# Kernel optimization log

Measured on AMD Instinct MI355X. Metric: run time of the kernel, lower is better.

## Reference

```python
import jax, jax.numpy as jnp
import numpy as np

T, D, E, F, K = 2048, 1024, 16, 512, 2  # tokens, hidden, experts, expert d_ff, top_k
NORM_TOPK = True


def setup_inputs() -> dict:
    key = jax.random.key(0)
    k0, k1, k2, k3 = jax.random.split(key, 4)
    hidden_states = jax.random.normal(k0, (T, D), jnp.float32)
    w_gate = jax.random.normal(k1, (E, D), jnp.float32) * (D ** -0.5)      # router Linear(D, E), no bias
    w13 = jax.random.normal(k2, (E, 2 * F, D), jnp.float32) * (D ** -0.5)  # fused gate+up proj per expert
    w2 = jax.random.normal(k3, (E, D, F), jnp.float32) * (F ** -0.5)       # down proj per expert
    return {"hidden_states": hidden_states, "w_gate": w_gate, "w13": w13, "w2": w2}


def reference(hidden_states, w_gate, w13, w2):
    # Router: softmax (fp32) -> top-k -> optional renorm
    logits = hidden_states @ w_gate.T                                   # [T, E]
    probs = jax.nn.softmax(logits.astype(jnp.float32), axis=-1)
    weights, selected = jax.lax.top_k(probs, K)                          # [T, K]
    if NORM_TOPK:
        weights = weights / jnp.sum(weights, axis=-1, keepdims=True)
    weights = weights.astype(hidden_states.dtype)

    # Sparse combine matrix: combine[t, e] = routing weight iff expert e selected for token t
    combine = jnp.zeros((T, E), hidden_states.dtype)
    combine = combine.at[jnp.arange(T)[:, None], selected].add(weights)

    # Expert FFN (computed for all experts, zeroed by combine; faithful math)
    h = jnp.einsum('td,efd->tef', hidden_states, w13)                    # [T, E, 2F]
    gate, up = jnp.split(h, 2, axis=-1)
    act = jax.nn.silu(gate) * up                                         # SiluAndMul, [T, E, F]
    y = jnp.einsum('tef,edf->ted', act, w2)                              # [T, E, D]
    return jnp.einsum('ted,te->td', y, combine)                          # [T, D]
```

## Files before the change

### kernel.cpp

```cpp
#include <hip/hip_runtime.h>
#include <hip/hip_bf16.h>
#include <math.h>

#define T_TOK 2048
#define DIM   1024
#define NEXP  16
#define FDIM  512
#define TOPK  2

#define BM 128
#define BN 64
#define BK 32

typedef float f32x4 __attribute__((ext_vector_type(4)));
typedef short s16x8 __attribute__((ext_vector_type(8)));

static __device__ __forceinline__ ushort f2bf(float f) {
  union { float f; unsigned u; } v; v.f = f;
  unsigned u = v.u;
  unsigned r = u + 0x7fffu + ((u >> 16) & 1u);
  return (ushort)(r >> 16);
}
static __device__ __forceinline__ float bf2f(ushort h) {
  union { unsigned u; float f; } v; v.u = ((unsigned)h) << 16; return v.f;
}
static __device__ __forceinline__ void split2(float f, ushort& h, ushort& l) {
  ushort hb = f2bf(f);
  h = hb;
  l = f2bf(f - bf2f(hb));
}

__global__ __launch_bounds__(64) void router_k(const float* __restrict__ x,
                                               const float* __restrict__ wg,
                                               int* __restrict__ sel,
                                               float* __restrict__ wt,
                                               int* __restrict__ cnt) {
  int t = blockIdx.x;
  int lane = threadIdx.x;
  const float* xr = x + (size_t)t * DIM;
  float acc[NEXP];
#pragma unroll
  for (int e = 0; e < NEXP; ++e) acc[e] = 0.f;
  for (int d0 = 0; d0 < DIM; d0 += 64) {
    float xv = xr[d0 + lane];
#pragma unroll
    for (int e = 0; e < NEXP; ++e) acc[e] += xv * wg[e * DIM + d0 + lane];
  }
#pragma unroll
  for (int e = 0; e < NEXP; ++e) {
    float v = acc[e];
    v += __shfl_xor(v, 32); v += __shfl_xor(v, 16); v += __shfl_xor(v, 8);
    v += __shfl_xor(v, 4);  v += __shfl_xor(v, 2);  v += __shfl_xor(v, 1);
    acc[e] = v;
  }
  if (lane == 0) {
    float b1 = -1e30f, b2 = -1e30f; int i1 = 0, i2 = 0;
#pragma unroll
    for (int e = 0; e < NEXP; ++e) {
      float v = acc[e];
      if (v > b1) { b2 = b1; i2 = i1; b1 = v; i1 = e; }
      else if (v > b2) { b2 = v; i2 = e; }
    }
    float r = expf(b2 - b1);
    float w2v = r / (1.f + r);
    float w1v = 1.f - w2v;
    sel[t * 2 + 0] = i1; sel[t * 2 + 1] = i2;
    wt[t * 2 + 0] = w1v; wt[t * 2 + 1] = w2v;
    atomicAdd(&cnt[i1], 1);
    atomicAdd(&cnt[i2], 1);
  }
}

__global__ __launch_bounds__(256) void xsplit_k(const float* __restrict__ x,
                                                ushort* __restrict__ xhi,
                                                ushort* __restrict__ xlo) {
  int idx = (blockIdx.x * 256 + threadIdx.x) * 4;
  float4 v = *(const float4*)(x + idx);
  ushort h0,h1,h2,h3,l0,l1,l2,l3;
  split2(v.x, h0, l0); split2(v.y, h1, l1);
  split2(v.z, h2, l2); split2(v.w, h3, l3);
  *(ushort4*)(xhi + idx) = make_ushort4(h0, h1, h2, h3);
  *(ushort4*)(xlo + idx) = make_ushort4(l0, l1, l2, l3);
}

__global__ void offsets_k(const int* __restrict__ cnt, int* __restrict__ off) {
  if (threadIdx.x == 0 && blockIdx.x == 0) {
    int s = 0;
#pragma unroll
    for (int e = 0; e < NEXP; ++e) { off[e] = s; s += cnt[e]; }
    off[NEXP] = s;
  }
}

__global__ __launch_bounds__(256) void fill_k(const int* __restrict__ sel,
                                              const float* __restrict__ wt,
                                              const int* __restrict__ off,
                                              int* __restrict__ cnt2,
                                              int* __restrict__ rowtok,
                                              float* __restrict__ rowwt) {
  int i = blockIdx.x * 256 + threadIdx.x;
  if (i >= T_TOK * TOPK) return;
  int e = sel[i];
  int pos = off[e] + atomicAdd(&cnt2[e], 1);
  rowtok[pos] = i >> 1;
  rowwt[pos] = wt[i];
}

#define DECL_SET(S) uint4 pAh0##S, pAl0##S, pAh1##S, pAl1##S; float4 pB0##S, pB1##S;

#define LOAD_SET(S, KB)                                                      \
  pAh0##S = *(const uint4*)(a0h + (KB)); pAl0##S = *(const uint4*)(a0l + (KB)); \
  pAh1##S = *(const uint4*)(a1h + (KB)); pAl1##S = *(const uint4*)(a1l + (KB)); \
  pB0##S = *(const float4*)(bsrc + (KB)); pB1##S = *(const float4*)(bsrc + (KB) + 4);

#define MOE_KSTEP(S, KS, NSv)                                                \
  do {                                                                       \
    asm volatile("s_waitcnt lgkmcnt(0)" ::: "memory");   \
    __builtin_amdgcn_s_barrier();               \
    __builtin_amdgcn_sched_barrier(0);                                       \
    *(uint4*)((char*)Ah + boA0) = pAh0##S;                                   \
    *(uint4*)((char*)Al + boA0) = pAl0##S;                                   \
    *(uint4*)((char*)Ah + boA1) = pAh1##S;                                   \
    *(uint4*)((char*)Al + boA1) = pAl1##S;                                   \
    {                                                                        \
      float fv[8] = {pB0##S.x, pB0##S.y, pB0##S.z, pB0##S.w,                 \
                     pB1##S.x, pB1##S.y, pB1##S.z, pB1##S.w};                \
      uint hp[4], lp[4];                                                     \
      _Pragma("unroll")                                                      \
      for (int j = 0; j < 4; ++j) {                                          \
        ushort ha, la, hb, lb;                                               \
        split2(fv[2 * j], ha, la);                                           \
        split2(fv[2 * j + 1], hb, lb);                                       \
        hp[j] = (uint)ha | ((uint)hb << 16);                                 \
        lp[j] = (uint)la | ((uint)lb << 16);                                 \
      }                                                                      \
      *(uint4*)((char*)Bh + boB) = make_uint4(hp[0], hp[1], hp[2], hp[3]);   \
      *(uint4*)((char*)Bl + boB) = make_uint4(lp[0], lp[1], lp[2], lp[3]);   \
    }                                                                        \
    if ((KS) + 2 < (NSv)) { int kb = ((KS) + 2) * BK; LOAD_SET(S, kb) }      \
    asm volatile("s_waitcnt lgkmcnt(0)" ::: "memory");  \
    __builtin_amdgcn_s_barrier();             \
    __builtin_amdgcn_sched_barrier(0);                                       \
    s16x8 ah[4], al[4], bh[2], bl[2];                                        \
    _Pragma("unroll")                                                        \
    for (int fm = 0; fm < 4; ++fm) {                                         \
      int row = wm + fm * 16 + lr;                                           \
      int bo = (row * 64 + lk * 16) ^ ((row & 7) << 4);                      \
      ah[fm] = *(const s16x8*)((char*)Ah + bo);                              \
      al[fm] = *(const s16x8*)((char*)Al + bo);                              \
    }                                                                        \
    _Pragma("unroll")                                                        \
    for (int fn = 0; fn < 2; ++fn) {                                         \
      int row = wn + fn * 16 + lr;                                           \
      int bo = (row * 64 + lk * 16) ^ ((row & 7) << 4);                      \
      bh[fn] = *(const s16x8*)((char*)Bh + bo);                              \
      bl[fn] = *(const s16x8*)((char*)Bl + bo);                              \
    }                                                                        \
    _Pragma("unroll")                                                        \
    for (int fm = 0; fm < 4; ++fm)                                           \
      _Pragma("unroll")                                                      \
      for (int fn = 0; fn < 2; ++fn) {                                       \
        acc[fm][fn] = __builtin_amdgcn_mfma_f32_16x16x32_bf16(ah[fm], bh[fn], acc[fm][fn], 0, 0, 0); \
        acc[fm][fn] = __builtin_amdgcn_mfma_f32_16x16x32_bf16(ah[fm], bl[fn], acc[fm][fn], 0, 0, 0); \
        acc[fm][fn] = __builtin_amdgcn_mfma_f32_16x16x32_bf16(al[fm], bh[fn], acc[fm][fn], 0, 0, 0); \
      }                                                                      \
  } while (0)

__global__ __launch_bounds__(256, 2) void gemm1_k(const ushort* __restrict__ xhi,
                                                  const ushort* __restrict__ xlo,
                                                  const float* __restrict__ w13,
                                                  const int* __restrict__ off,
                                                  const int* __restrict__ rowtok,
                                                  float* __restrict__ H) {
  int e = blockIdx.z;
  int rbeg = off[e];
  int rows = off[e + 1] - rbeg;
  int m0 = blockIdx.y * BM;
  if (m0 >= rows) return;
  int n0 = blockIdx.x * BN;

  __shared__ ushort Ah[BM * BK], Al[BM * BK], Bh[BN * BK], Bl[BN * BK];
  __shared__ int toksh[BM];

  int tid = threadIdx.x;
  if (tid < BM) {
    int r = m0 + tid;
    toksh[tid] = rowtok[rbeg + (r < rows ? r : rows - 1)];
  }
  __syncthreads();

  int srow = tid >> 2;
  int sc = tid & 3;
  int tok0 = toksh[srow];
  int tok1 = toksh[srow + 64];
  const ushort* a0h = xhi + (size_t)tok0 * DIM + sc * 8;
  const ushort* a0l = xlo + (size_t)tok0 * DIM + sc * 8;
  const ushort* a1h = xhi + (size_t)tok1 * DIM + sc * 8;
  const ushort* a1l = xlo + (size_t)tok1 * DIM + sc * 8;
  const float*  bsrc = w13 + ((size_t)e * (2 * FDIM) + (n0 + srow)) * DIM + sc * 8;

  int boA0 = (srow * 64 + sc * 16) ^ ((srow & 7) << 4);
  int boA1 = ((srow + 64) * 64 + sc * 16) ^ ((srow & 7) << 4);
  int boB  = boA0;

  f32x4 acc[4][2];
#pragma unroll
  for (int a = 0; a < 4; ++a)
#pragma unroll
    for (int b = 0; b < 2; ++b) acc[a][b] = {0.f, 0.f, 0.f, 0.f};

  int lane = tid & 63;
  int w = tid >> 6;
  int wm = (w & 1) * 64, wn = (w >> 1) * 32;
  int lr = lane & 15, lk = lane >> 4;

  DECL_SET(_A) DECL_SET(_B)
  LOAD_SET(_A, 0)
  LOAD_SET(_B, BK)

  const int NS = DIM / BK;
  for (int ks = 0; ks < NS; ks += 2) {
    MOE_KSTEP(_A, ks, NS);
    MOE_KSTEP(_B, ks + 1, NS);
  }

#pragma unroll
  for (int fm = 0; fm < 4; ++fm) {
    int rloc = wm + fm * 16 + lk * 4;
#pragma unroll
    for (int j = 0; j < 4; ++j) {
      int row = rloc + j;
      if (m0 + row < rows) {
        size_t gr = (size_t)(rbeg + m0 + row) * (2 * FDIM);
#pragma unroll
        for (int fn = 0; fn < 2; ++fn)
          H[gr + n0 + wn + fn * 16 + lr] = acc[fm][fn][j];
      }
    }
  }
}

__global__ __launch_bounds__(256) void act_k(const float* __restrict__ H,
                                             ushort* __restrict__ ahi,
                                             ushort* __restrict__ alo) {
  int idx = (blockIdx.x * 256 + threadIdx.x) * 4;
  int r = idx >> 9;
  int f = idx & 511;
  const float* hrow = H + (size_t)r * (2 * FDIM);
  float4 g = *(const float4*)(hrow + f);
  float4 u = *(const float4*)(hrow + FDIM + f);
  float a0 = g.x / (1.f + expf(-g.x)) * u.x;
  float a1 = g.y / (1.f + expf(-g.y)) * u.y;
  float a2 = g.z / (1.f + expf(-g.z)) * u.z;
  float a3 = g.w / (1.f + expf(-g.w)) * u.w;
  ushort h0,h1,h2,h3,l0,l1,l2,l3;
  split2(a0, h0, l0); split2(a1, h1, l1);
  split2(a2, h2, l2); split2(a3, h3, l3);
  *(ushort4*)(ahi + (size_t)r * FDIM + f) = make_ushort4(h0, h1, h2, h3);
  *(ushort4*)(alo + (size_t)r * FDIM + f) = make_ushort4(l0, l1, l2, l3);
}

__global__ __launch_bounds__(256, 2) void gemm2_k(const ushort* __restrict__ ahi,
                                                  const ushort* __restrict__ alo,
                                                  const float* __restrict__ w2,
                                                  const int* __restrict__ off,
                                                  const int* __restrict__ rowtok,
                                                  const float* __restrict__ rowwt,
                                                  float* __restrict__ out) {
  int e = blockIdx.z;
  int rbeg = off[e];
  int rows = off[e + 1] - rbeg;
  int m0 = blockIdx.y * BM;
  if (m0 >= rows) return;
  int n0 = blockIdx.x * BN;

  __shared__ ushort Ah[BM * BK], Al[BM * BK], Bh[BN * BK], Bl[BN * BK];
  __shared__ int toksh[BM];
  __shared__ float wtsh[BM];

  int tid = threadIdx.x;
  if (tid < BM) {
    int r = m0 + tid;
    int rr = rbeg + (r < rows ? r : rows - 1);
    toksh[tid] = rowtok[rr];
    wtsh[tid] = (r < rows) ? rowwt[rr] : 0.f;
  }
  __syncthreads();

  int srow = tid >> 2;
  int sc = tid & 3;
  int rg0 = m0 + srow;       rg0 = (rg0 < rows ? rg0 : rows - 1);
  int rg1 = m0 + srow + 64;  rg1 = (rg1 < rows ? rg1 : rows - 1);
  const ushort* a0h = ahi + (size_t)(rbeg + rg0) * FDIM + sc * 8;
  const ushort* a0l = alo + (size_t)(rbeg + rg0) * FDIM + sc * 8;
  const ushort* a1h = ahi + (size_t)(rbeg + rg1) * FDIM + sc * 8;
  const ushort* a1l = alo + (size_t)(rbeg + rg1) * FDIM + sc * 8;
  const float*  bsrc = w2 + ((size_t)e * DIM + (n0 + srow)) * FDIM + sc * 8;

  int boA0 = (srow * 64 + sc * 16) ^ ((srow & 7) << 4);
  int boA1 = ((srow + 64) * 64 + sc * 16) ^ ((srow & 7) << 4);
  int boB  = boA0;

  f32x4 acc[4][2];
#pragma unroll
  for (int a = 0; a < 4; ++a)
#pragma unroll
    for (int b = 0; b < 2; ++b) acc[a][b] = {0.f, 0.f, 0.f, 0.f};

  int lane = tid & 63;
  int w = tid >> 6;
  int wm = (w & 1) * 64, wn = (w >> 1) * 32;
  int lr = lane & 15, lk = lane >> 4;

  DECL_SET(_A) DECL_SET(_B)
  LOAD_SET(_A, 0)
  LOAD_SET(_B, BK)

  const int NS = FDIM / BK;
  for (int ks = 0; ks < NS; ks += 2) {
    MOE_KSTEP(_A, ks, NS);
    MOE_KSTEP(_B, ks + 1, NS);
  }

#pragma unroll
  for (int fm = 0; fm < 4; ++fm) {
    int rloc = wm + fm * 16 + lk * 4;
#pragma unroll
    for (int j = 0; j < 4; ++j) {
      int row = rloc + j;
      if (m0 + row < rows) {
        int tok = toksh[row];
        float wgt = wtsh[row];
        float* orow = out + (size_t)tok * DIM + n0;
#pragma unroll
        for (int fn = 0; fn < 2; ++fn)
          atomicAdd(orow + wn + fn * 16 + lr, wgt * acc[fm][fn][j]);
      }
    }
  }
}

extern "C" void kernel_launch(void* const* d_in, const int* in_sizes, int n_in,
                              void* d_out, int out_size, void* d_ws, size_t ws_size,
                              hipStream_t stream) {
  const float* x   = (const float*)d_in[0];
  const float* wg  = (const float*)d_in[1];
  const float* w13 = (const float*)d_in[2];
  const float* w2  = (const float*)d_in[3];
  float* out = (float*)d_out;

  char* ws = (char*)d_ws;
  int*   cnt    = (int*)(ws + 0);
  int*   cnt2   = (int*)(ws + 64);
  int*   off    = (int*)(ws + 128);
  int*   sel    = (int*)(ws + 1024);
  float* wt     = (float*)(ws + 1024 + 16384);
  int*   rowtok = (int*)(ws + 1024 + 32768);
  float* rowwt  = (float*)(ws + 1024 + 49152);
  size_t o = 128 * 1024;
  ushort* xhi = (ushort*)(ws + o); o += (size_t)T_TOK * DIM * 2;
  ushort* xlo = (ushort*)(ws + o); o += (size_t)T_TOK * DIM * 2;
  float*  H   = (float*)(ws + o);  o += (size_t)T_TOK * TOPK * 2 * FDIM * 4;
  ushort* ahi = (ushort*)(ws + o); o += (size_t)T_TOK * TOPK * FDIM * 2;
  ushort* alo = (ushort*)(ws + o); o += (size_t)T_TOK * TOPK * FDIM * 2;

  hipMemsetAsync(ws, 0, 256, stream);
  hipMemsetAsync(d_out, 0, (size_t)out_size * sizeof(float), stream);

  router_k<<<T_TOK, 64, 0, stream>>>(x, wg, sel, wt, cnt);
  xsplit_k<<<(T_TOK * DIM) / 1024, 256, 0, stream>>>(x, xhi, xlo);
  offsets_k<<<1, 64, 0, stream>>>(cnt, off);
  fill_k<<<(T_TOK * TOPK + 255) / 256, 256, 0, stream>>>(sel, wt, off, cnt2, rowtok, rowwt);

  dim3 g1(2 * FDIM / BN, T_TOK / BM, NEXP);
  gemm1_k<<<g1, 256, 0, stream>>>(xhi, xlo, w13, off, rowtok, H);

  act_k<<<(T_TOK * TOPK * FDIM) / 1024, 256, 0, stream>>>(H, ahi, alo);

  dim3 g2(DIM / BN, T_TOK / BM, NEXP);
  gemm2_k<<<g2, 256, 0, stream>>>(ahi, alo, w2, off, rowtok, rowwt, out);
}
```

Before: 293.6 us.

## Load MFMA operands directly from global memory, removing LDS staging and barriers

Both expert GEMMs stop staging A and B tiles through shared memory with barriers. Each lane now loads its MFMA fragments straight from global memory into registers, with a register-level multi-buffer prefetch: two stages for A and four for B. The fp32 weights are split into bf16 hi and lo parts in registers just before the MFMAs. This removes LDS traffic and synchronisation, but it also gives up the data reuse across waves that the shared tiles provided, so global and L2 load traffic rises and register pressure grows. The first GSTEP definition (with a bl1 typo) is immediately undefined and replaced, and the gemm2 epilogue now reads token ids and routing weights from global memory instead of shared memory.

```diff
diff --git a/kernel.cpp b/kernel.cpp
--- a/kernel.cpp
+++ b/kernel.cpp
@@ -28,6 +28,25 @@
   ushort hb = f2bf(f);
   h = hb;
   l = f2bf(f - bf2f(hb));
+}
+
+union u4s8 { uint4 u; s16x8 s; };
+static __device__ __forceinline__ s16x8 as8(uint4 v) { u4s8 c; c.u = v; return c.s; }
+
+static __device__ __forceinline__ void conv8(float4 f0, float4 f1, s16x8& h, s16x8& l) {
+  float fs[8] = {f0.x, f0.y, f0.z, f0.w, f1.x, f1.y, f1.z, f1.w};
+  uint hp[4], lp[4];
+#pragma unroll
+  for (int j = 0; j < 4; ++j) {
+    ushort ha, la, hb, lb;
+    split2(fs[2 * j], ha, la);
+    split2(fs[2 * j + 1], hb, lb);
+    hp[j] = (uint)ha | ((uint)hb << 16);
+    lp[j] = (uint)la | ((uint)lb << 16);
+  }
+  uint4 hu = make_uint4(hp[0], hp[1], hp[2], hp[3]);
+  uint4 lu = make_uint4(lp[0], lp[1], lp[2], lp[3]);
+  h = as8(hu); l = as8(lu);
 }
 
 __global__ __launch_bounds__(64) void router_k(const float* __restrict__ x,
@@ -106,65 +125,64 @@
   rowwt[pos] = wt[i];
 }
 
-#define DECL_SET(S) uint4 pAh0##S, pAl0##S, pAh1##S, pAl1##S; float4 pB0##S, pB1##S;
-
-#define LOAD_SET(S, KB)                                                      \
-  pAh0##S = *(const uint4*)(a0h + (KB)); pAl0##S = *(const uint4*)(a0l + (KB)); \
-  pAh1##S = *(const uint4*)(a1h + (KB)); pAl1##S = *(const uint4*)(a1l + (KB)); \
-  pB0##S = *(const float4*)(bsrc + (KB)); pB1##S = *(const float4*)(bsrc + (KB) + 4);
-
-#define MOE_KSTEP(S, KS, NSv)                                                \
-  do {                                                                       \
-    asm volatile("s_waitcnt lgkmcnt(0)" ::: "memory");   \
-    __builtin_amdgcn_s_barrier();               \
-    __builtin_amdgcn_sched_barrier(0);                                       \
-    *(uint4*)((char*)Ah + boA0) = pAh0##S;                                   \
-    *(uint4*)((char*)Al + boA0) = pAl0##S;                                   \
-    *(uint4*)((char*)Ah + boA1) = pAh1##S;                                   \
-    *(uint4*)((char*)Al + boA1) = pAl1##S;                                   \
-    {                                                                        \
-      float fv[8] = {pB0##S.x, pB0##S.y, pB0##S.z, pB0##S.w,                 \
-                     pB1##S.x, pB1##S.y, pB1##S.z, pB1##S.w};                \
-      uint hp[4], lp[4];                                                     \
-      _Pragma("unroll")                                                      \
-      for (int j = 0; j < 4; ++j) {                                          \
-        ushort ha, la, hb, lb;                                               \
-        split2(fv[2 * j], ha, la);                                           \
-        split2(fv[2 * j + 1], hb, lb);                                       \
-        hp[j] = (uint)ha | ((uint)hb << 16);                                 \
-        lp[j] = (uint)la | ((uint)lb << 16);                                 \
-      }                                                                      \
-      *(uint4*)((char*)Bh + boB) = make_uint4(hp[0], hp[1], hp[2], hp[3]);   \
-      *(uint4*)((char*)Bl + boB) = make_uint4(lp[0], lp[1], lp[2], lp[3]);   \
-    }                                                                        \
-    if ((KS) + 2 < (NSv)) { int kb = ((KS) + 2) * BK; LOAD_SET(S, kb) }      \
-    asm volatile("s_waitcnt lgkmcnt(0)" ::: "memory");  \
-    __builtin_amdgcn_s_barrier();             \
-    __builtin_amdgcn_sched_barrier(0);                                       \
-    s16x8 ah[4], al[4], bh[2], bl[2];                                        \
-    _Pragma("unroll")                                                        \
-    for (int fm = 0; fm < 4; ++fm) {                                         \
-      int row = wm + fm * 16 + lr;                                           \
-      int bo = (row * 64 + lk * 16) ^ ((row & 7) << 4);                      \
-      ah[fm] = *(const s16x8*)((char*)Ah + bo);                              \
-      al[fm] = *(const s16x8*)((char*)Al + bo);                              \
-    }                                                                        \
-    _Pragma("unroll")                                                        \
-    for (int fn = 0; fn < 2; ++fn) {                                         \
-      int row = wn + fn * 16 + lr;                                           \
-      int bo = (row * 64 + lk * 16) ^ ((row & 7) << 4);                      \
-      bh[fn] = *(const s16x8*)((char*)Bh + bo);                              \
-      bl[fn] = *(const s16x8*)((char*)Bl + bo);                              \
-    }                                                                        \
-    _Pragma("unroll")                                                        \
-    for (int fm = 0; fm < 4; ++fm)                                           \
-      _Pragma("unroll")                                                      \
-      for (int fn = 0; fn < 2; ++fn) {                                       \
-        acc[fm][fn] = __builtin_amdgcn_mfma_f32_16x16x32_bf16(ah[fm], bh[fn], acc[fm][fn], 0, 0, 0); \
-        acc[fm][fn] = __builtin_amdgcn_mfma_f32_16x16x32_bf16(ah[fm], bl[fn], acc[fm][fn], 0, 0, 0); \
-        acc[fm][fn] = __builtin_amdgcn_mfma_f32_16x16x32_bf16(al[fm], bh[fn], acc[fm][fn], 0, 0, 0); \
-      }                                                                      \
-  } while (0)
+#define DECL_SETS                                                            \
+  uint4 aH00,aH10,aH20,aH30, aL00,aL10,aL20,aL30;                            \
+  uint4 aH01,aH11,aH21,aH31, aL01,aL11,aL21,aL31;                            \
+  float4 w000,w010,w100,w110;                                                \
+  float4 w001,w011,w101,w111;                                                \
+  float4 w002,w012,w102,w112;                                                \
+  float4 w003,w013,w103,w113;
+
+#define LOAD_A(S, KB) do { int kk = (KB); kk = kk <= AKMAX ? kk : AKMAX;     \
+  aH0##S = *(const uint4*)(pAH[0] + kk); aH1##S = *(const uint4*)(pAH[1] + kk); \
+  aH2##S = *(const uint4*)(pAH[2] + kk); aH3##S = *(const uint4*)(pAH[3] + kk); \
+  aL0##S = *(const uint4*)(pAL[0] + kk); aL1##S = *(const uint4*)(pAL[1] + kk); \
+  aL2##S = *(const uint4*)(pAL[2] + kk); aL3##S = *(const uint4*)(pAL[3] + kk); \
+} while (0)
+
+#define LOAD_B(S, KB) do { int kk = (KB); kk = kk <= AKMAX ? kk : AKMAX;     \
+  w00##S = *(const float4*)(pB0 + kk); w01##S = *(const float4*)(pB0 + kk + 4); \
+  w10##S = *(const float4*)(pB1 + kk); w11##S = *(const float4*)(pB1 + kk + 4); \
+} while (0)
+
+#define GSTEP(AS, BS, KS) do {                                               \
+  s16x8 bh0, bl0, bh1, bl1;                                                  \
+  conv8(w00##BS, w01##BS, bh0, bl0);                                         \
+  conv8(w10##BS, w11##BS, bh1, bl1);                                         \
+  LOAD_B(BS, ((KS) + 4) * BK);               \
+  s16x8 ah[4] = {as8(aH0##AS), as8(aH1##AS), as8(aH2##AS), as8(aH3##AS)};    \
+  s16x8 al[4] = {as8(aL0##AS), as8(aL1##AS), as8(aL2##AS), as8(aL3##AS)};    \
+  _Pragma("unroll")                                                          \
+  for (int fm = 0; fm < 4; ++fm) {                                           \
+    acc[fm][0] = __builtin_amdgcn_mfma_f32_16x16x32_bf16(ah[fm], bh0, acc[fm][0], 0, 0, 0); \
+    acc[fm][0] = __builtin_amdgcn_mfma_f32_16x16x32_bf16(ah[fm], bl0, acc[fm][0], 0, 0, 0); \
+    acc[fm][0] = __builtin_amdgcn_mfma_f32_16x16x32_bf16(al[fm], bh0, acc[fm][0], 0, 0, 0); \
+    acc[fm][1] = __builtin_amdgcn_mfma_f32_16x16x32_bf16(ah[fm], bh1, acc[fm][1], 0, 0, 0); \
+    acc[fm][1] = __builtin_amdgcn_mfma_f32_16x16x32_bf16(ah[fm], bl1, acc[fm][1], 0, 0, 0); \
+    acc[fm][1] = __builtin_amdgcn_mfma_f32_16x16x32_bf16(al[fm], bl1 , acc[fm][1], 0, 0, 0); \
+  }                                                                          \
+  LOAD_A(AS, ((KS) + 2) * BK);                  \
+} while (0)
+
+#undef GSTEP
+#define GSTEP(AS, BS, KS) do {                                               \
+  s16x8 bh0, bl0, bh1, bl1;                                                  \
+  conv8(w00##BS, w01##BS, bh0, bl0);                                         \
+  conv8(w10##BS, w11##BS, bh1, bl1);                                         \
+  LOAD_B(BS, ((KS) + 4) * BK);                                               \
+  s16x8 ah[4] = {as8(aH0##AS), as8(aH1##AS), as8(aH2##AS), as8(aH3##AS)};    \
+  s16x8 al[4] = {as8(aL0##AS), as8(aL1##AS), as8(aL2##AS), as8(aL3##AS)};    \
+  _Pragma("unroll")                                                          \
+  for (int fm = 0; fm < 4; ++fm) {                                           \
+    acc[fm][0] = __builtin_amdgcn_mfma_f32_16x16x32_bf16(ah[fm], bh0, acc[fm][0], 0, 0, 0); \
+    acc[fm][0] = __builtin_amdgcn_mfma_f32_16x16x32_bf16(ah[fm], bl0, acc[fm][0], 0, 0, 0); \
+    acc[fm][0] = __builtin_amdgcn_mfma_f32_16x16x32_bf16(al[fm], bh0, acc[fm][0], 0, 0, 0); \
+    acc[fm][1] = __builtin_amdgcn_mfma_f32_16x16x32_bf16(ah[fm], bh1, acc[fm][1], 0, 0, 0); \
+    acc[fm][1] = __builtin_amdgcn_mfma_f32_16x16x32_bf16(ah[fm], bl1, acc[fm][1], 0, 0, 0); \
+    acc[fm][1] = __builtin_amdgcn_mfma_f32_16x16x32_bf16(al[fm], bh1, acc[fm][1], 0, 0, 0); \
+  }                                                                          \
+  LOAD_A(AS, ((KS) + 2) * BK);                                               \
+} while (0)
 
 __global__ __launch_bounds__(256, 2) void gemm1_k(const ushort* __restrict__ xhi,
                                                   const ushort* __restrict__ xlo,
@@ -172,6 +190,7 @@
                                                   const int* __restrict__ off,
                                                   const int* __restrict__ rowtok,
                                                   float* __restrict__ H) {
+  enum { NS = DIM / BK, AKMAX = (NS - 1) * BK };
   int e = blockIdx.z;
   int rbeg = off[e];
   int rows = off[e + 1] - rbeg;
@@ -179,49 +198,39 @@
   if (m0 >= rows) return;
   int n0 = blockIdx.x * BN;
 
-  __shared__ ushort Ah[BM * BK], Al[BM * BK], Bh[BN * BK], Bl[BN * BK];
-  __shared__ int toksh[BM];
-
   int tid = threadIdx.x;
-  if (tid < BM) {
-    int r = m0 + tid;
-    toksh[tid] = rowtok[rbeg + (r < rows ? r : rows - 1)];
-  }
-  __syncthreads();
-
-  int srow = tid >> 2;
-  int sc = tid & 3;
-  int tok0 = toksh[srow];
-  int tok1 = toksh[srow + 64];
-  const ushort* a0h = xhi + (size_t)tok0 * DIM + sc * 8;
-  const ushort* a0l = xlo + (size_t)tok0 * DIM + sc * 8;
-  const ushort* a1h = xhi + (size_t)tok1 * DIM + sc * 8;
-  const ushort* a1l = xlo + (size_t)tok1 * DIM + sc * 8;
-  const float*  bsrc = w13 + ((size_t)e * (2 * FDIM) + (n0 + srow)) * DIM + sc * 8;
-
-  int boA0 = (srow * 64 + sc * 16) ^ ((srow & 7) << 4);
-  int boA1 = ((srow + 64) * 64 + sc * 16) ^ ((srow & 7) << 4);
-  int boB  = boA0;
-
-  f32x4 acc[4][2];
-#pragma unroll
-  for (int a = 0; a < 4; ++a)
-#pragma unroll
-    for (int b = 0; b < 2; ++b) acc[a][b] = {0.f, 0.f, 0.f, 0.f};
-
   int lane = tid & 63;
   int w = tid >> 6;
   int wm = (w & 1) * 64, wn = (w >> 1) * 32;
   int lr = lane & 15, lk = lane >> 4;
 
-  DECL_SET(_A) DECL_SET(_B)
-  LOAD_SET(_A, 0)
-  LOAD_SET(_B, BK)
-
-  const int NS = DIM / BK;
-  for (int ks = 0; ks < NS; ks += 2) {
-    MOE_KSTEP(_A, ks, NS);
-    MOE_KSTEP(_B, ks + 1, NS);
+  const ushort* pAH[4]; const ushort* pAL[4];
+#pragma unroll
+  for (int fm = 0; fm < 4; ++fm) {
+    int row = m0 + wm + fm * 16 + lr;
+    row = row < rows ? row : rows - 1;
+    int tok = rowtok[rbeg + row];
+    size_t o = (size_t)tok * DIM + lk * 8;
+    pAH[fm] = xhi + o; pAL[fm] = xlo + o;
+  }
+  const float* pB0 = w13 + ((size_t)e * (2 * FDIM) + (n0 + wn + lr)) * DIM + lk * 8;
+  const float* pB1 = pB0 + (size_t)16 * DIM;
+
+  f32x4 acc[4][2];
+#pragma unroll
+  for (int a = 0; a < 4; ++a)
+#pragma unroll
+    for (int b = 0; b < 2; ++b) acc[a][b] = {0.f, 0.f, 0.f, 0.f};
+
+  DECL_SETS
+  LOAD_A(0, 0); LOAD_A(1, BK);
+  LOAD_B(0, 0); LOAD_B(1, BK); LOAD_B(2, 2 * BK); LOAD_B(3, 3 * BK);
+
+  for (int ks = 0; ks < NS; ks += 4) {
+    GSTEP(0, 0, ks);
+    GSTEP(1, 1, ks + 1);
+    GSTEP(0, 2, ks + 2);
+    GSTEP(1, 3, ks + 3);
   }
 
 #pragma unroll
@@ -267,6 +276,7 @@
                                                   const int* __restrict__ rowtok,
                                                   const float* __restrict__ rowwt,
                                                   float* __restrict__ out) {
+  enum { NS = FDIM / BK, AKMAX = (NS - 1) * BK };
   int e = blockIdx.z;
   int rbeg = off[e];
   int rows = off[e + 1] - rbeg;
@@ -274,52 +284,38 @@
   if (m0 >= rows) return;
   int n0 = blockIdx.x * BN;
 
-  __shared__ ushort Ah[BM * BK], Al[BM * BK], Bh[BN * BK], Bl[BN * BK];
-  __shared__ int toksh[BM];
-  __shared__ float wtsh[BM];
-
   int tid = threadIdx.x;
-  if (tid < BM) {
-    int r = m0 + tid;
-    int rr = rbeg + (r < rows ? r : rows - 1);
-    toksh[tid] = rowtok[rr];
-    wtsh[tid] = (r < rows) ? rowwt[rr] : 0.f;
-  }
-  __syncthreads();
-
-  int srow = tid >> 2;
-  int sc = tid & 3;
-  int rg0 = m0 + srow;       rg0 = (rg0 < rows ? rg0 : rows - 1);
-  int rg1 = m0 + srow + 64;  rg1 = (rg1 < rows ? rg1 : rows - 1);
-  const ushort* a0h = ahi + (size_t)(rbeg + rg0) * FDIM + sc * 8;
-  const ushort* a0l = alo + (size_t)(rbeg + rg0) * FDIM + sc * 8;
-  const ushort* a1h = ahi + (size_t)(rbeg + rg1) * FDIM + sc * 8;
-  const ushort* a1l = alo + (size_t)(rbeg + rg1) * FDIM + sc * 8;
-  const float*  bsrc = w2 + ((size_t)e * DIM + (n0 + srow)) * FDIM + sc * 8;
-
-  int boA0 = (srow * 64 + sc * 16) ^ ((srow & 7) << 4);
-  int boA1 = ((srow + 64) * 64 + sc * 16) ^ ((srow & 7) << 4);
-  int boB  = boA0;
-
-  f32x4 acc[4][2];
-#pragma unroll
-  for (int a = 0; a < 4; ++a)
-#pragma unroll
-    for (int b = 0; b < 2; ++b) acc[a][b] = {0.f, 0.f, 0.f, 0.f};
-
   int lane = tid & 63;
   int w = tid >> 6;
   int wm = (w & 1) * 64, wn = (w >> 1) * 32;
   int lr = lane & 15, lk = lane >> 4;
 
-  DECL_SET(_A) DECL_SET(_B)
-  LOAD_SET(_A, 0)
-  LOAD_SET(_B, BK)
-
-  const int NS = FDIM / BK;
-  for (int ks = 0; ks < NS; ks += 2) {
-    MOE_KSTEP(_A, ks, NS);
-    MOE_KSTEP(_B, ks + 1, NS);
+  const ushort* pAH[4]; const ushort* pAL[4];
+#pragma unroll
+  for (int fm = 0; fm < 4; ++fm) {
+    int row = m0 + wm + fm * 16 + lr;
+    row = row < rows ? row : rows - 1;
+    size_t o = (size_t)(rbeg + row) * FDIM + lk * 8;
+    pAH[fm] = ahi + o; pAL[fm] = alo + o;
+  }
+  const float* pB0 = w2 + ((size_t)e * DIM + (n0 + wn + lr)) * FDIM + lk * 8;
+  const float* pB1 = pB0 + (size_t)16 * FDIM;
+
+  f32x4 acc[4][2];
+#pragma unroll
+  for (int a = 0; a < 4; ++a)
+#pragma unroll
+    for (int b = 0; b < 2; ++b) acc[a][b] = {0.f, 0.f, 0.f, 0.f};
+
+  DECL_SETS
+  LOAD_A(0, 0); LOAD_A(1, BK);
+  LOAD_B(0, 0); LOAD_B(1, BK); LOAD_B(2, 2 * BK); LOAD_B(3, 3 * BK);
+
+  for (int ks = 0; ks < NS; ks += 4) {
+    GSTEP(0, 0, ks);
+    GSTEP(1, 1, ks + 1);
+    GSTEP(0, 2, ks + 2);
+    GSTEP(1, 3, ks + 3);
   }
 
 #pragma unroll
@@ -329,8 +325,9 @@
     for (int j = 0; j < 4; ++j) {
       int row = rloc + j;
       if (m0 + row < rows) {
-        int tok = toksh[row];
-        float wgt = wtsh[row];
+        int idx = rbeg + m0 + row;
+        int tok = rowtok[idx];
+        float wgt = rowwt[idx];
         float* orow = out + (size_t)tok * DIM + n0;
 #pragma unroll
         for (int fn = 0; fn < 2; ++fn)
```

New measurement: 749.5 us. 155% more time.
